# Optimization experiments

Hardware: AMD Instinct MI355X
Metric: run time of the kernel (lower is better)

## Reference

```python
import jax, jax.numpy as jnp
import numpy as np
from jax import lax

B, T = 64, 200
NUM_C, DIM_S, SIZE_M = 2000, 128, 50


def setup_inputs() -> dict:
    key = jax.random.key(0)
    ks = jax.random.split(key, 12)
    d = {}
    d['skill'] = jax.random.randint(ks[0], (B, T), 0, NUM_C)
    d['answer'] = jax.random.randint(ks[1], (B, T), 0, 2)
    s = 1.0 / np.sqrt(DIM_S)
    d['k_emb'] = jax.random.normal(ks[2], (NUM_C + 1, DIM_S), jnp.float32)
    d['v_emb'] = jax.random.normal(ks[3], (2 * NUM_C + 1, DIM_S), jnp.float32)
    # kaiming_normal on [size_m, dim_s]: std = sqrt(2/dim_s)
    d['Mk'] = jax.random.normal(ks[4], (SIZE_M, DIM_S), jnp.float32) * np.sqrt(2.0 / DIM_S)
    d['Mv0'] = jax.random.normal(ks[5], (SIZE_M, DIM_S), jnp.float32) * np.sqrt(2.0 / DIM_S)
    d['f_W'] = jax.random.normal(ks[6], (DIM_S, 2 * DIM_S), jnp.float32) * (1.0 / np.sqrt(2 * DIM_S))
    d['f_b'] = jnp.zeros((DIM_S,), jnp.float32)
    d['p_W'] = jax.random.normal(ks[7], (NUM_C, DIM_S), jnp.float32) * s
    d['p_b'] = jnp.zeros((NUM_C,), jnp.float32)
    d['e_W'] = jax.random.normal(ks[8], (DIM_S, DIM_S), jnp.float32) * s
    d['e_b'] = jnp.zeros((DIM_S,), jnp.float32)
    d['a_W'] = jax.random.normal(ks[9], (DIM_S, DIM_S), jnp.float32) * s
    d['a_b'] = jnp.zeros((DIM_S,), jnp.float32)
    return d


def reference(skill, answer, k_emb, v_emb, Mk, Mv0, f_W, f_b, p_W, p_b, e_W, e_b, a_W, a_b):
    num_c = p_W.shape[0]
    bsz = skill.shape[0]
    answer_x = jnp.where(answer == 2, 1, answer)
    x = skill + num_c * answer_x                       # [B,T]
    k = k_emb[skill]                                   # [B,T,D]
    v = v_emb[x]                                       # [B,T,D]
    w = jax.nn.softmax(jnp.einsum('btd,md->btm', k, Mk), axis=-1)   # [B,T,M]
    e = jax.nn.sigmoid(jnp.einsum('btd,ed->bte', v, e_W) + e_b)      # [B,T,D]
    a = jnp.tanh(jnp.einsum('btd,ed->bte', v, a_W) + a_b)            # [B,T,D]

    Mv_init = jnp.broadcast_to(Mv0, (bsz,) + Mv0.shape)              # [B,M,D]

    def step(Mvt, inp):
        et, at, wt = inp                               # [B,D],[B,D],[B,M]
        # read uses pre-update memory (Mv[:, :-1] in the torch code)
        read = jnp.einsum('bm,bmd->bd', wt, Mvt)
        Mvt_new = Mvt * (1.0 - wt[:, :, None] * et[:, None, :]) + wt[:, :, None] * at[:, None, :]
        return Mvt_new, read

    _, reads = lax.scan(step, Mv_init,
                        (e.transpose(1, 0, 2), a.transpose(1, 0, 2), w.transpose(1, 0, 2)))
    reads = reads.transpose(1, 0, 2)                   # [B,T,D]

    f = jnp.tanh(jnp.concatenate([reads, k], axis=-1) @ f_W.T + f_b)  # [B,T,D]
    p = jax.nn.sigmoid(f @ p_W.T + p_b)                # [B,T,num_c] (dropout is identity at eval)
    p = p[:, :-1, :]
    next_skill = skill[:, 1:]                          # [B,T-1]
    idx = jnp.minimum(next_skill, num_c - 1)
    pred = jnp.take_along_axis(p, idx[..., None], axis=-1)[..., 0]
    pred = jnp.where(next_skill < num_c, pred, 0.0)    # index num_c -> zero row in torch one_hot
    return pred
```

## Files before the change

kernel.cpp:

```cpp
#include <hip/hip_runtime.h>
#include <math.h>

#define Bsz 64
#define Tn 200
#define NUMC 2000
#define DS 128
#define SM 50
#define NTOK (Bsz*Tn)
#define WG2 10
#define MPG2 5

typedef __attribute__((ext_vector_type(8))) short bfrag;
typedef __attribute__((ext_vector_type(4))) float f32x4;
typedef __attribute__((ext_vector_type(4))) unsigned int u32x4;

__device__ __forceinline__ unsigned short f2bf(float x) {
    unsigned int u = __builtin_bit_cast(unsigned int, x);
    u = u + 0x7fffu + ((u >> 16) & 1u);
    return (unsigned short)(u >> 16);
}
__device__ __forceinline__ unsigned int pack2(float a, float b) {
    return (unsigned int)f2bf(a) | ((unsigned int)f2bf(b) << 16);
}
__device__ __forceinline__ bfrag mk_frag(f32x4 x, f32x4 y) {
    u32x4 t;
    t[0] = pack2(x[0], x[1]); t[1] = pack2(x[2], x[3]);
    t[2] = pack2(y[0], y[1]); t[3] = pack2(y[2], y[3]);
    return __builtin_bit_cast(bfrag, t);
}

__device__ __forceinline__ float fast_exp(float x)  { return __builtin_amdgcn_exp2f(x * 1.44269504f); }
__device__ __forceinline__ float fast_rcp(float x)  { return __builtin_amdgcn_rcpf(x); }
__device__ __forceinline__ float fast_sigmoid(float x) { return fast_rcp(1.f + fast_exp(-x)); }
__device__ __forceinline__ float fast_tanh(float x) { return 1.f - 2.f * fast_rcp(fast_exp(2.f * x) + 1.f); }

__device__ __forceinline__ void load_group(const bfrag* __restrict__ B, int nt0, int L, bfrag bf[4][4]) {
    #pragma unroll
    for (int t = 0; t < 4; t++)
        #pragma unroll
        for (int ki = 0; ki < 4; ki++)
            bf[t][ki] = B[(size_t)((nt0 + t) * 4 + ki) * 64 + L];
}
__device__ __forceinline__ void mfma_group(const bfrag A[4], const bfrag bf[4][4], f32x4 acc[4]) {
    #pragma unroll
    for (int ki = 0; ki < 4; ki++)
        #pragma unroll
        for (int t = 0; t < 4; t++)
            acc[t] = __builtin_amdgcn_mfma_f32_16x16x32_bf16(A[ki], bf[t][ki], acc[t], 0, 0, 0);
}

__global__ __launch_bounds__(256) void k0_cast(
    const float* __restrict__ eW, const float* __restrict__ aW,
    const float* __restrict__ fW, const float* __restrict__ Mk,
    unsigned int* __restrict__ BeaU, unsigned int* __restrict__ BkmU,
    unsigned int* __restrict__ Bf0U)
{
    const int g = blockIdx.x * 256 + threadIdx.x;
    if (g >= 9216) return;
    int gm, mat;
    unsigned int* dst;
    if (g < 4096)      { mat = 0; gm = g;        dst = BeaU; }
    else if (g < 7168) { mat = 1; gm = g - 4096; dst = BkmU; }
    else               { mat = 2; gm = g - 7168; dst = Bf0U; }
    const int nt = gm >> 8, r = gm & 255, ki = r >> 6, L = r & 63;
    const int n = nt * 16 + (L & 15);
    const int k = ki * 32 + (L >> 4) * 8;

    const float* src = nullptr;
    if (mat == 0) {
        src = (n < 128) ? (eW + (size_t)n * DS + k) : (aW + (size_t)(n - 128) * DS + k);
    } else if (mat == 1) {
        if (n < 128)      src = fW + (size_t)n * (2 * DS) + DS + k;
        else if (n < 128 + SM) src = Mk + (size_t)(n - 128) * DS + k;
    } else {
        src = fW + (size_t)n * (2 * DS) + k;
    }
    float v[8];
    #pragma unroll
    for (int j = 0; j < 8; j++) v[j] = src ? src[j] : 0.f;
    u32x4 o;
    o[0] = pack2(v[0], v[1]); o[1] = pack2(v[2], v[3]);
    o[2] = pack2(v[4], v[5]); o[3] = pack2(v[6], v[7]);
    ((u32x4*)dst)[gm] = o;
}

__global__ __launch_bounds__(64) void k1_gemm(
    const int* __restrict__ skill, const int* __restrict__ answer,
    const float* __restrict__ k_emb, const float* __restrict__ v_emb,
    const unsigned int* __restrict__ BeaU, const unsigned int* __restrict__ BkmU,
    const float* __restrict__ eB, const float* __restrict__ aB,
    float* __restrict__ w_buf, float* __restrict__ e_buf,
    float* __restrict__ a_buf, float* __restrict__ kp_buf)
{
    const int bid = blockIdx.x;
    const int L = threadIdx.x, L15 = L & 15, quad = L >> 4;

    if (bid < NTOK/16) {
        const int tok0 = bid * 16;
        const int tokA = tok0 + L15;
        const int tokD0 = tok0 + quad * 4;

        const bfrag* Bea = (const bfrag*)BeaU;
        bfrag bfA[4][4], bfB[4][4];
        load_group(Bea, 0, L, bfA);
        load_group(Bea, 4, L, bfB);

        const int s  = skill[tokA];
        const int an = answer[tokA];
        const int ax = (an == 2) ? 1 : an;
        const float* vp = v_emb + ((size_t)(s + NUMC * ax)) * DS + quad * 8;
        bfrag Vf[4];
        #pragma unroll
        for (int ki = 0; ki < 4; ki++) {
            const f32x4* a = (const f32x4*)(vp + ki * 32);
            Vf[ki] = mk_frag(a[0], a[1]);
        }

        f32x4 acc[4];
        #pragma unroll
        for (int t = 0; t < 4; t++) acc[t] = (f32x4){0.f,0.f,0.f,0.f};
        mfma_group(Vf, bfA, acc);
        load_group(Bea, 8, L, bfA);
        #pragma unroll
        for (int t = 0; t < 4; t++) {
            const int n = t * 16 + L15;
            const float bias = eB[n];
            #pragma unroll
            for (int reg = 0; reg < 4; reg++)
                e_buf[(size_t)(tokD0 + reg) * DS + n] = fast_sigmoid(acc[t][reg] + bias);
        }

        #pragma unroll
        for (int t = 0; t < 4; t++) acc[t] = (f32x4){0.f,0.f,0.f,0.f};
        mfma_group(Vf, bfB, acc);
        load_group(Bea, 12, L, bfB);
        #pragma unroll
        for (int t = 0; t < 4; t++) {
            const int n = (4 + t) * 16 + L15;
            const float bias = eB[n];
            #pragma unroll
            for (int reg = 0; reg < 4; reg++)
                e_buf[(size_t)(tokD0 + reg) * DS + n] = fast_sigmoid(acc[t][reg] + bias);
        }

        #pragma unroll
        for (int t = 0; t < 4; t++) acc[t] = (f32x4){0.f,0.f,0.f,0.f};
        mfma_group(Vf, bfA, acc);
        #pragma unroll
        for (int t = 0; t < 4; t++) {
            const int n = t * 16 + L15;
            const float bias = aB[n];
            #pragma unroll
            for (int reg = 0; reg < 4; reg++)
                a_buf[(size_t)(tokD0 + reg) * DS + n] = fast_tanh(acc[t][reg] + bias);
        }

        #pragma unroll
        for (int t = 0; t < 4; t++) acc[t] = (f32x4){0.f,0.f,0.f,0.f};
        mfma_group(Vf, bfB, acc);
        #pragma unroll
        for (int t = 0; t < 4; t++) {
            const int n = (4 + t) * 16 + L15;
            const float bias = aB[n];
            #pragma unroll
            for (int reg = 0; reg < 4; reg++)
                a_buf[(size_t)(tokD0 + reg) * DS + n] = fast_tanh(acc[t][reg] + bias);
        }
    } else {
        const int tok0 = (bid - NTOK/16) * 16;
        const int tokA = tok0 + L15;
        const int tokD0 = tok0 + quad * 4;

        const bfrag* Bkm = (const bfrag*)BkmU;
        bfrag bfA[4][4], bfB[4][4];
        load_group(Bkm, 0, L, bfA);
        load_group(Bkm, 4, L, bfB);

        const int s = skill[tokA];
        const float* kp = k_emb + (size_t)s * DS + quad * 8;
        bfrag Kf[4];
        #pragma unroll
        for (int ki = 0; ki < 4; ki++) {
            const f32x4* b = (const f32x4*)(kp + ki * 32);
            Kf[ki] = mk_frag(b[0], b[1]);
        }

        __shared__ float wl[16][52];

        f32x4 acc[4];
        #pragma unroll
        for (int t = 0; t < 4; t++) acc[t] = (f32x4){0.f,0.f,0.f,0.f};
        mfma_group(Kf, bfA, acc);
        load_group(Bkm, 8, L, bfA);
        #pragma unroll
        for (int t = 0; t < 4; t++) {
            const int n = t * 16 + L15;
            #pragma unroll
            for (int reg = 0; reg < 4; reg++)
                kp_buf[(size_t)(tokD0 + reg) * DS + n] = acc[t][reg];
        }

        #pragma unroll
        for (int t = 0; t < 4; t++) acc[t] = (f32x4){0.f,0.f,0.f,0.f};
        mfma_group(Kf, bfB, acc);
        #pragma unroll
        for (int t = 0; t < 4; t++) {
            const int n = (4 + t) * 16 + L15;
            #pragma unroll
            for (int reg = 0; reg < 4; reg++)
                kp_buf[(size_t)(tokD0 + reg) * DS + n] = acc[t][reg];
        }

        #pragma unroll
        for (int t = 0; t < 4; t++) acc[t] = (f32x4){0.f,0.f,0.f,0.f};
        mfma_group(Kf, bfA, acc);
        #pragma unroll
        for (int t = 0; t < 4; t++) {
            const int c = (8 + t) * 16 + L15 - 128;
            if (c < SM) {
                #pragma unroll
                for (int reg = 0; reg < 4; reg++)
                    wl[quad * 4 + reg][c] = acc[t][reg];
            }
        }
        __syncthreads();
        if (L < 16) {
            float mx = -1e30f;
            for (int m = 0; m < SM; m++) mx = fmaxf(mx, wl[L][m]);
            float sum = 0.f;
            float ex[SM];
            for (int m = 0; m < SM; m++) { ex[m] = fast_exp(wl[L][m] - mx); sum += ex[m]; }
            const float inv = fast_rcp(sum);
            float* wp = w_buf + (size_t)(tok0 + L) * SM;
            for (int m = 0; m < SM; m++) wp[m] = ex[m] * inv;
        }
    }
}

__global__ __launch_bounds__(64) void k2_scan(
    const float* __restrict__ w_buf, const float* __restrict__ e_buf,
    const float* __restrict__ a_buf, const float* __restrict__ Mv0,
    float* __restrict__ part_buf)
{
    const int bi   = blockIdx.x;
    const int b    = bi / (2*WG2);
    const int r    = bi % (2*WG2);
    const int dh   = r / WG2;
    const int mg   = r % WG2;
    const int lane = threadIdx.x;
    const int d    = dh*64 + lane;
    const int m0   = mg * MPG2;
    const int base = b * Tn;

    float Mv[MPG2];
    #pragma unroll
    for (int m = 0; m < MPG2; m++) Mv[m] = Mv0[(size_t)(m0+m)*DS + d];

    float* pout = part_buf + (size_t)mg * NTOK * DS;

    float se[4][2], sa[4][2], sw[4][2][MPG2];

    #define LOADST(ST, T)                                                      \
        { const int tc_ = ((T) < Tn) ? (T) : 0;                                \
          _Pragma("unroll")                                                    \
          for (int q_ = 0; q_ < 2; q_++) {                                     \
              const int tf_ = base + tc_ + q_;                                 \
              se[ST][q_] = e_buf[(size_t)tf_*DS + d];                          \
              sa[ST][q_] = a_buf[(size_t)tf_*DS + d];                          \
              _Pragma("unroll")                                                \
              for (int m_ = 0; m_ < MPG2; m_++)                                \
                  sw[ST][q_][m_] = w_buf[(size_t)tf_*SM + m0 + m_];            \
          } }

    LOADST(0, 0) LOADST(1, 2) LOADST(2, 4) LOADST(3, 6)

    for (int i = 0; i < 25; i++) {
        const int tb = i * 8;
        #pragma unroll
        for (int sub = 0; sub < 4; sub++) {
            const int t0 = tb + sub * 2;
            #pragma unroll
            for (int q = 0; q < 2; q++) {
                const float ev = se[sub][q], av = sa[sub][q];
                float rd = 0.f;
                #pragma unroll
                for (int m = 0; m < MPG2; m++) {
                    const float wm = sw[sub][q][m];
                    rd = fmaf(wm, Mv[m], rd);
                    Mv[m] = fmaf(-wm, fmaf(ev, Mv[m], -av), Mv[m]);
                }
                pout[(size_t)(base + t0 + q)*DS + d] = rd;
            }
            LOADST(sub, t0 + 8)
        }
    }
}

__global__ __launch_bounds__(64) void k3_gemm(
    const float* __restrict__ part_buf, const float* __restrict__ kp_buf,
    const unsigned int* __restrict__ Bf0U, const float* __restrict__ fB,
    const float* __restrict__ pW, const float* __restrict__ pB,
    const int* __restrict__ skill, float* __restrict__ out)
{
    const int L = threadIdx.x, L15 = L & 15, quad = L >> 4;
    const int tok0 = blockIdx.x * 16;
    const int tokA = tok0 + L15;
    const int tokD0 = tok0 + quad * 4;

    const bfrag* Bf0 = (const bfrag*)Bf0U;
    bfrag bfA[4][4], bfB[4][4];
    load_group(Bf0, 0, L, bfA);
    load_group(Bf0, 4, L, bfB);

    bfrag Rf[4];
    #pragma unroll
    for (int ki = 0; ki < 4; ki++) {
        const float* p0 = part_buf + (size_t)tokA * DS + ki * 32 + quad * 8;
        f32x4 x = (f32x4){0.f,0.f,0.f,0.f}, y = (f32x4){0.f,0.f,0.f,0.f};
        #pragma unroll
        for (int g = 0; g < WG2; g++) {
            const f32x4* q4 = (const f32x4*)(p0 + (size_t)g * NTOK * DS);
            x = x + q4[0]; y = y + q4[1];
        }
        Rf[ki] = mk_frag(x, y);
    }

    float f[4][8];
    f32x4 acc[4];

    #pragma unroll
    for (int t = 0; t < 4; t++) acc[t] = (f32x4){0.f,0.f,0.f,0.f};
    mfma_group(Rf, bfA, acc);
    #pragma unroll
    for (int t = 0; t < 4; t++) {
        const int n = t * 16 + L15;
        const float fb = fB[n];
        #pragma unroll
        for (int reg = 0; reg < 4; reg++)
            f[reg][t] = fast_tanh(acc[t][reg] + kp_buf[(size_t)(tokD0 + reg) * DS + n] + fb);
    }

    #pragma unroll
    for (int t = 0; t < 4; t++) acc[t] = (f32x4){0.f,0.f,0.f,0.f};
    mfma_group(Rf, bfB, acc);
    #pragma unroll
    for (int t = 0; t < 4; t++) {
        const int n = (4 + t) * 16 + L15;
        const float fb = fB[n];
        #pragma unroll
        for (int reg = 0; reg < 4; reg++)
            f[reg][4 + t] = fast_tanh(acc[t][reg] + kp_buf[(size_t)(tokD0 + reg) * DS + n] + fb);
    }

    #pragma unroll
    for (int reg = 0; reg < 4; reg++) {
        const int tok = tokD0 + reg;
        const int t = tok % Tn;
        const bool act = (t < Tn - 1);
        int sn = 0, ix = 0;
        float contrib = 0.f;
        if (act) {
            sn = skill[tok + 1];
            ix = (sn < NUMC) ? sn : (NUMC - 1);
            const float* pr = pW + (size_t)ix * DS + L15;
            #pragma unroll
            for (int nt = 0; nt < 8; nt++)
                contrib = fmaf(f[reg][nt], pr[nt * 16], contrib);
        }
        #pragma unroll
        for (int msk = 1; msk <= 8; msk <<= 1)
            contrib += __shfl_xor(contrib, msk);
        if (act && L15 == 0) {
            const float val = contrib + pB[ix];
            const float prd = (sn < NUMC) ? fast_sigmoid(val) : 0.f;
            out[(size_t)(tok / Tn) * (Tn - 1) + t] = prd;
        }
    }
}

extern "C" void kernel_launch(void* const* d_in, const int* in_sizes, int n_in,
                              void* d_out, int out_size, void* d_ws, size_t ws_size,
                              hipStream_t stream)
{
    const int*   skill  = (const int*)  d_in[0];
    const int*   answer = (const int*)  d_in[1];
    const float* k_emb  = (const float*)d_in[2];
    const float* v_emb  = (const float*)d_in[3];
    const float* Mk     = (const float*)d_in[4];
    const float* Mv0    = (const float*)d_in[5];
    const float* f_W    = (const float*)d_in[6];
    const float* f_b    = (const float*)d_in[7];
    const float* p_W    = (const float*)d_in[8];
    const float* p_b    = (const float*)d_in[9];
    const float* e_W    = (const float*)d_in[10];
    const float* e_b    = (const float*)d_in[11];
    const float* a_W    = (const float*)d_in[12];
    const float* a_b    = (const float*)d_in[13];
    float* out = (float*)d_out;

    float* ws       = (float*)d_ws;
    float* w_buf    = ws;
    float* e_buf    = w_buf    + (size_t)NTOK*SM;
    float* a_buf    = e_buf    + (size_t)NTOK*DS;
    float* kp_buf   = a_buf    + (size_t)NTOK*DS;
    float* part_buf = kp_buf   + (size_t)NTOK*DS;
    unsigned int* BeaU = (unsigned int*)(part_buf + (size_t)WG2*NTOK*DS);
    unsigned int* BkmU = BeaU + 4096 * 4;
    unsigned int* Bf0U = BkmU + 3072 * 4;

    k0_cast<<<36, 256, 0, stream>>>(e_W, a_W, f_W, Mk, BeaU, BkmU, Bf0U);
    k1_gemm<<<2*(NTOK/16), 64, 0, stream>>>(skill, answer, k_emb, v_emb,
        BeaU, BkmU, e_b, a_b, w_buf, e_buf, a_buf, kp_buf);
    k2_scan<<<Bsz*2*WG2, 64, 0, stream>>>(w_buf, e_buf, a_buf, Mv0, part_buf);
    k3_gemm<<<NTOK/16, 64, 0, stream>>>(part_buf, kp_buf, Bf0U, f_b,
        p_W, p_b, skill, out);
}
```

Before: 140.6 us.

## Reduce scan partial reads in shared memory instead of global partial buffer

The scan kernel now packs the 10 memory-slot groups as waves of one workgroup (640 threads per batch/half) and sums their per-step read contributions through a shared-memory stash every 20 steps. Only the final reads go to global memory, so the 10x partial buffer and the 10-way reduction in the output GEMM kernel are gone. In exchange the scan gains two __syncthreads per chunk, which couple the waves, and there are fewer, larger workgroups, which may hurt latency hiding.

```diff
diff --git a/kernel.cpp b/kernel.cpp
--- a/kernel.cpp
+++ b/kernel.cpp
@@ -7,8 +7,9 @@
 #define DS 128
 #define SM 50
 #define NTOK (Bsz*Tn)
-#define WG2 10
-#define MPG2 5
+#define MPG 5
+#define NWV 10
+#define CH 20
 
 typedef __attribute__((ext_vector_type(8))) short bfrag;
 typedef __attribute__((ext_vector_type(4))) float f32x4;
@@ -237,28 +238,26 @@
     }
 }
 
-__global__ __launch_bounds__(64) void k2_scan(
+__global__ __launch_bounds__(64*NWV) void k2_scan(
     const float* __restrict__ w_buf, const float* __restrict__ e_buf,
     const float* __restrict__ a_buf, const float* __restrict__ Mv0,
-    float* __restrict__ part_buf)
+    float* __restrict__ reads_buf)
 {
-    const int bi   = blockIdx.x;
-    const int b    = bi / (2*WG2);
-    const int r    = bi % (2*WG2);
-    const int dh   = r / WG2;
-    const int mg   = r % WG2;
-    const int lane = threadIdx.x;
-    const int d    = dh*64 + lane;
-    const int m0   = mg * MPG2;
+    const int b    = blockIdx.x >> 1;
+    const int dh   = blockIdx.x & 1;
+    const int wave = threadIdx.x >> 6;
+    const int lane = threadIdx.x & 63;
+    const int d    = dh * 64 + lane;
+    const int m0   = wave * MPG;
     const int base = b * Tn;
 
-    float Mv[MPG2];
-    #pragma unroll
-    for (int m = 0; m < MPG2; m++) Mv[m] = Mv0[(size_t)(m0+m)*DS + d];
-
-    float* pout = part_buf + (size_t)mg * NTOK * DS;
-
-    float se[4][2], sa[4][2], sw[4][2][MPG2];
+    __shared__ float stash[NWV][CH][64];
+
+    float Mv[MPG];
+    #pragma unroll
+    for (int m = 0; m < MPG; m++) Mv[m] = Mv0[(size_t)(m0+m)*DS + d];
+
+    float se[4][2], sa[4][2], sw[4][2][MPG];
 
     #define LOADST(ST, T)                                                      \
         { const int tc_ = ((T) < Tn) ? (T) : 0;                                \
@@ -268,36 +267,48 @@
               se[ST][q_] = e_buf[(size_t)tf_*DS + d];                          \
               sa[ST][q_] = a_buf[(size_t)tf_*DS + d];                          \
               _Pragma("unroll")                                                \
-              for (int m_ = 0; m_ < MPG2; m_++)                                \
+              for (int m_ = 0; m_ < MPG; m_++)                                 \
                   sw[ST][q_][m_] = w_buf[(size_t)tf_*SM + m0 + m_];            \
           } }
 
     LOADST(0, 0) LOADST(1, 2) LOADST(2, 4) LOADST(3, 6)
 
-    for (int i = 0; i < 25; i++) {
-        const int tb = i * 8;
-        #pragma unroll
-        for (int sub = 0; sub < 4; sub++) {
-            const int t0 = tb + sub * 2;
+    for (int c = 0; c < Tn/CH; c++) {
+        #pragma unroll
+        for (int s = 0; s < CH/2; s++) {
+            const int t0 = c*CH + s*2;
+            const int st = (c*(CH/2) + s) & 3;
             #pragma unroll
             for (int q = 0; q < 2; q++) {
-                const float ev = se[sub][q], av = sa[sub][q];
+                const float ev = se[st][q], av = sa[st][q];
                 float rd = 0.f;
                 #pragma unroll
-                for (int m = 0; m < MPG2; m++) {
-                    const float wm = sw[sub][q][m];
+                for (int m = 0; m < MPG; m++) {
+                    const float wm = sw[st][q][m];
                     rd = fmaf(wm, Mv[m], rd);
                     Mv[m] = fmaf(-wm, fmaf(ev, Mv[m], -av), Mv[m]);
                 }
-                pout[(size_t)(base + t0 + q)*DS + d] = rd;
+                stash[wave][s*2+q][lane] = rd;
             }
-            LOADST(sub, t0 + 8)
-        }
-    }
+            LOADST(st, t0 + 8)
+        }
+        __syncthreads();
+        #pragma unroll
+        for (int q = 0; q < 2; q++) {
+            const int slot = threadIdx.x + q * (64*NWV);
+            const int tl = slot >> 6, dl = slot & 63;
+            float sum = 0.f;
+            #pragma unroll
+            for (int g = 0; g < NWV; g++) sum += stash[g][tl][dl];
+            reads_buf[(size_t)(base + c*CH + tl)*DS + dh*64 + dl] = sum;
+        }
+        __syncthreads();
+    }
+    #undef LOADST
 }
 
 __global__ __launch_bounds__(64) void k3_gemm(
-    const float* __restrict__ part_buf, const float* __restrict__ kp_buf,
+    const float* __restrict__ reads_buf, const float* __restrict__ kp_buf,
     const unsigned int* __restrict__ Bf0U, const float* __restrict__ fB,
     const float* __restrict__ pW, const float* __restrict__ pB,
     const int* __restrict__ skill, float* __restrict__ out)
@@ -315,14 +326,8 @@
     bfrag Rf[4];
     #pragma unroll
     for (int ki = 0; ki < 4; ki++) {
-        const float* p0 = part_buf + (size_t)tokA * DS + ki * 32 + quad * 8;
-        f32x4 x = (f32x4){0.f,0.f,0.f,0.f}, y = (f32x4){0.f,0.f,0.f,0.f};
-        #pragma unroll
-        for (int g = 0; g < WG2; g++) {
-            const f32x4* q4 = (const f32x4*)(p0 + (size_t)g * NTOK * DS);
-            x = x + q4[0]; y = y + q4[1];
-        }
-        Rf[ki] = mk_frag(x, y);
+        const f32x4* q4 = (const f32x4*)(reads_buf + (size_t)tokA * DS + ki * 32 + quad * 8);
+        Rf[ki] = mk_frag(q4[0], q4[1]);
     }
 
     float f[4][8];
@@ -398,20 +403,20 @@
     const float* a_b    = (const float*)d_in[13];
     float* out = (float*)d_out;
 
-    float* ws       = (float*)d_ws;
-    float* w_buf    = ws;
-    float* e_buf    = w_buf    + (size_t)NTOK*SM;
-    float* a_buf    = e_buf    + (size_t)NTOK*DS;
-    float* kp_buf   = a_buf    + (size_t)NTOK*DS;
-    float* part_buf = kp_buf   + (size_t)NTOK*DS;
-    unsigned int* BeaU = (unsigned int*)(part_buf + (size_t)WG2*NTOK*DS);
+    float* ws        = (float*)d_ws;
+    float* w_buf     = ws;
+    float* e_buf     = w_buf     + (size_t)NTOK*SM;
+    float* a_buf     = e_buf     + (size_t)NTOK*DS;
+    float* kp_buf    = a_buf     + (size_t)NTOK*DS;
+    float* reads_buf = kp_buf    + (size_t)NTOK*DS;
+    unsigned int* BeaU = (unsigned int*)(reads_buf + (size_t)NTOK*DS);
     unsigned int* BkmU = BeaU + 4096 * 4;
     unsigned int* Bf0U = BkmU + 3072 * 4;
 
     k0_cast<<<36, 256, 0, stream>>>(e_W, a_W, f_W, Mk, BeaU, BkmU, Bf0U);
     k1_gemm<<<2*(NTOK/16), 64, 0, stream>>>(skill, answer, k_emb, v_emb,
         BeaU, BkmU, e_b, a_b, w_buf, e_buf, a_buf, kp_buf);
-    k2_scan<<<Bsz*2*WG2, 64, 0, stream>>>(w_buf, e_buf, a_buf, Mv0, part_buf);
-    k3_gemm<<<NTOK/16, 64, 0, stream>>>(part_buf, kp_buf, Bf0U, f_b,
+    k2_scan<<<Bsz*2, 64*NWV, 0, stream>>>(w_buf, e_buf, a_buf, Mv0, reads_buf);
+    k3_gemm<<<NTOK/16, 64, 0, stream>>>(reads_buf, kp_buf, Bf0U, f_b,
         p_W, p_b, skill, out);
 }
```

Result: slower. 294.8 us (+109.7%).

## Drop weight pre-cast kernel and store scan partial reads in bf16

Applied to the files above, without the earlier changes.

Removes the k0_cast launch that pre-packed weights into bf16 fragment layout. Each GEMM block now loads fp32 weights directly and converts them in registers. The scan kernel also writes its 10 per-group partial read sums as bf16 instead of fp32, halving that intermediate traffic, and k3 widens and sums them. This saves a launch and a large chunk of workspace bandwidth, at the cost of redundant per-block weight conversion, twice the weight load bytes, and some precision lost on the partial sums.

```diff
diff --git a/kernel.cpp b/kernel.cpp
--- a/kernel.cpp
+++ b/kernel.cpp
@@ -22,6 +22,9 @@
 __device__ __forceinline__ unsigned int pack2(float a, float b) {
     return (unsigned int)f2bf(a) | ((unsigned int)f2bf(b) << 16);
 }
+__device__ __forceinline__ float bf2f(unsigned int u) {
+    return __builtin_bit_cast(float, u << 16);
+}
 __device__ __forceinline__ bfrag mk_frag(f32x4 x, f32x4 y) {
     u32x4 t;
     t[0] = pack2(x[0], x[1]); t[1] = pack2(x[2], x[3]);
@@ -34,12 +37,53 @@
 __device__ __forceinline__ float fast_sigmoid(float x) { return fast_rcp(1.f + fast_exp(-x)); }
 __device__ __forceinline__ float fast_tanh(float x) { return 1.f - 2.f * fast_rcp(fast_exp(2.f * x) + 1.f); }
 
-__device__ __forceinline__ void load_group(const bfrag* __restrict__ B, int nt0, int L, bfrag bf[4][4]) {
-    #pragma unroll
-    for (int t = 0; t < 4; t++)
-        #pragma unroll
-        for (int ki = 0; ki < 4; ki++)
-            bf[t][ki] = B[(size_t)((nt0 + t) * 4 + ki) * 64 + L];
+__device__ __forceinline__ void load_group_ea(
+    const float* __restrict__ eW, const float* __restrict__ aW,
+    int nt0, int L15, int quad, bfrag bf[4][4])
+{
+    #pragma unroll
+    for (int t = 0; t < 4; t++) {
+        const int n = (nt0 + t) * 16 + L15;
+        const float* row = (n < 128) ? (eW + (size_t)n * DS) : (aW + (size_t)(n - 128) * DS);
+        #pragma unroll
+        for (int ki = 0; ki < 4; ki++) {
+            const float* p = row + ki * 32 + quad * 8;
+            bf[t][ki] = mk_frag(*(const f32x4*)p, *(const f32x4*)(p + 4));
+        }
+    }
+}
+__device__ __forceinline__ void load_group_km(
+    const float* __restrict__ fW, const float* __restrict__ Mk,
+    int nt0, int L15, int quad, bfrag bf[4][4])
+{
+    #pragma unroll
+    for (int t = 0; t < 4; t++) {
+        const int n = (nt0 + t) * 16 + L15;
+        const bool valid = n < 128 + SM;
+        const float* row = (n < 128) ? (fW + (size_t)n * (2*DS) + DS)
+                                     : (Mk + (size_t)(n - 128) * DS);
+        #pragma unroll
+        for (int ki = 0; ki < 4; ki++) {
+            const float* p = row + ki * 32 + quad * 8;
+            f32x4 x = valid ? *(const f32x4*)p       : (f32x4){0.f,0.f,0.f,0.f};
+            f32x4 y = valid ? *(const f32x4*)(p + 4) : (f32x4){0.f,0.f,0.f,0.f};
+            bf[t][ki] = mk_frag(x, y);
+        }
+    }
+}
+__device__ __forceinline__ void load_group_f0(
+    const float* __restrict__ fW, int nt0, int L15, int quad, bfrag bf[4][4])
+{
+    #pragma unroll
+    for (int t = 0; t < 4; t++) {
+        const int n = (nt0 + t) * 16 + L15;
+        const float* row = fW + (size_t)n * (2*DS);
+        #pragma unroll
+        for (int ki = 0; ki < 4; ki++) {
+            const float* p = row + ki * 32 + quad * 8;
+            bf[t][ki] = mk_frag(*(const f32x4*)p, *(const f32x4*)(p + 4));
+        }
+    }
 }
 __device__ __forceinline__ void mfma_group(const bfrag A[4], const bfrag bf[4][4], f32x4 acc[4]) {
     #pragma unroll
@@ -47,47 +91,13 @@
         #pragma unroll
         for (int t = 0; t < 4; t++)
             acc[t] = __builtin_amdgcn_mfma_f32_16x16x32_bf16(A[ki], bf[t][ki], acc[t], 0, 0, 0);
-}
-
-__global__ __launch_bounds__(256) void k0_cast(
-    const float* __restrict__ eW, const float* __restrict__ aW,
-    const float* __restrict__ fW, const float* __restrict__ Mk,
-    unsigned int* __restrict__ BeaU, unsigned int* __restrict__ BkmU,
-    unsigned int* __restrict__ Bf0U)
-{
-    const int g = blockIdx.x * 256 + threadIdx.x;
-    if (g >= 9216) return;
-    int gm, mat;
-    unsigned int* dst;
-    if (g < 4096)      { mat = 0; gm = g;        dst = BeaU; }
-    else if (g < 7168) { mat = 1; gm = g - 4096; dst = BkmU; }
-    else               { mat = 2; gm = g - 7168; dst = Bf0U; }
-    const int nt = gm >> 8, r = gm & 255, ki = r >> 6, L = r & 63;
-    const int n = nt * 16 + (L & 15);
-    const int k = ki * 32 + (L >> 4) * 8;
-
-    const float* src = nullptr;
-    if (mat == 0) {
-        src = (n < 128) ? (eW + (size_t)n * DS + k) : (aW + (size_t)(n - 128) * DS + k);
-    } else if (mat == 1) {
-        if (n < 128)      src = fW + (size_t)n * (2 * DS) + DS + k;
-        else if (n < 128 + SM) src = Mk + (size_t)(n - 128) * DS + k;
-    } else {
-        src = fW + (size_t)n * (2 * DS) + k;
-    }
-    float v[8];
-    #pragma unroll
-    for (int j = 0; j < 8; j++) v[j] = src ? src[j] : 0.f;
-    u32x4 o;
-    o[0] = pack2(v[0], v[1]); o[1] = pack2(v[2], v[3]);
-    o[2] = pack2(v[4], v[5]); o[3] = pack2(v[6], v[7]);
-    ((u32x4*)dst)[gm] = o;
 }
 
 __global__ __launch_bounds__(64) void k1_gemm(
     const int* __restrict__ skill, const int* __restrict__ answer,
     const float* __restrict__ k_emb, const float* __restrict__ v_emb,
-    const unsigned int* __restrict__ BeaU, const unsigned int* __restrict__ BkmU,
+    const float* __restrict__ eW, const float* __restrict__ aW,
+    const float* __restrict__ fW, const float* __restrict__ Mk,
     const float* __restrict__ eB, const float* __restrict__ aB,
     float* __restrict__ w_buf, float* __restrict__ e_buf,
     float* __restrict__ a_buf, float* __restrict__ kp_buf)
@@ -100,10 +110,9 @@
         const int tokA = tok0 + L15;
         const int tokD0 = tok0 + quad * 4;
 
-        const bfrag* Bea = (const bfrag*)BeaU;
         bfrag bfA[4][4], bfB[4][4];
-        load_group(Bea, 0, L, bfA);
-        load_group(Bea, 4, L, bfB);
+        load_group_ea(eW, aW, 0, L15, quad, bfA);
+        load_group_ea(eW, aW, 4, L15, quad, bfB);
 
         const int s  = skill[tokA];
         const int an = answer[tokA];
@@ -120,7 +129,7 @@
         #pragma unroll
         for (int t = 0; t < 4; t++) acc[t] = (f32x4){0.f,0.f,0.f,0.f};
         mfma_group(Vf, bfA, acc);
-        load_group(Bea, 8, L, bfA);
+        load_group_ea(eW, aW, 8, L15, quad, bfA);
         #pragma unroll
         for (int t = 0; t < 4; t++) {
             const int n = t * 16 + L15;
@@ -133,7 +142,7 @@
         #pragma unroll
         for (int t = 0; t < 4; t++) acc[t] = (f32x4){0.f,0.f,0.f,0.f};
         mfma_group(Vf, bfB, acc);
-        load_group(Bea, 12, L, bfB);
+        load_group_ea(eW, aW, 12, L15, quad, bfB);
         #pragma unroll
         for (int t = 0; t < 4; t++) {
             const int n = (4 + t) * 16 + L15;
@@ -171,10 +180,9 @@
         const int tokA = tok0 + L15;
         const int tokD0 = tok0 + quad * 4;
 
-        const bfrag* Bkm = (const bfrag*)BkmU;
         bfrag bfA[4][4], bfB[4][4];
-        load_group(Bkm, 0, L, bfA);
-        load_group(Bkm, 4, L, bfB);
+        load_group_km(fW, Mk, 0, L15, quad, bfA);
+        load_group_km(fW, Mk, 4, L15, quad, bfB);
 
         const int s = skill[tokA];
         const float* kp = k_emb + (size_t)s * DS + quad * 8;
@@ -191,7 +199,7 @@
         #pragma unroll
         for (int t = 0; t < 4; t++) acc[t] = (f32x4){0.f,0.f,0.f,0.f};
         mfma_group(Kf, bfA, acc);
-        load_group(Bkm, 8, L, bfA);
+        load_group_km(fW, Mk, 8, L15, quad, bfA);
         #pragma unroll
         for (int t = 0; t < 4; t++) {
             const int n = t * 16 + L15;
@@ -240,7 +248,7 @@
 __global__ __launch_bounds__(64) void k2_scan(
     const float* __restrict__ w_buf, const float* __restrict__ e_buf,
     const float* __restrict__ a_buf, const float* __restrict__ Mv0,
-    float* __restrict__ part_buf)
+    unsigned short* __restrict__ part16)
 {
     const int bi   = blockIdx.x;
     const int b    = bi / (2*WG2);
@@ -256,7 +264,7 @@
     #pragma unroll
     for (int m = 0; m < MPG2; m++) Mv[m] = Mv0[(size_t)(m0+m)*DS + d];
 
-    float* pout = part_buf + (size_t)mg * NTOK * DS;
+    unsigned short* pout = part16 + (size_t)mg * NTOK * DS;
 
     float se[4][2], sa[4][2], sw[4][2][MPG2];
 
@@ -289,16 +297,17 @@
                     rd = fmaf(wm, Mv[m], rd);
                     Mv[m] = fmaf(-wm, fmaf(ev, Mv[m], -av), Mv[m]);
                 }
-                pout[(size_t)(base + t0 + q)*DS + d] = rd;
+                pout[(size_t)(base + t0 + q)*DS + d] = f2bf(rd);
             }
             LOADST(sub, t0 + 8)
         }
     }
+    #undef LOADST
 }
 
 __global__ __launch_bounds__(64) void k3_gemm(
-    const float* __restrict__ part_buf, const float* __restrict__ kp_buf,
-    const unsigned int* __restrict__ Bf0U, const float* __restrict__ fB,
+    const unsigned short* __restrict__ part16, const float* __restrict__ kp_buf,
+    const float* __restrict__ fW, const float* __restrict__ fB,
     const float* __restrict__ pW, const float* __restrict__ pB,
     const int* __restrict__ skill, float* __restrict__ out)
 {
@@ -307,22 +316,24 @@
     const int tokA = tok0 + L15;
     const int tokD0 = tok0 + quad * 4;
 
-    const bfrag* Bf0 = (const bfrag*)Bf0U;
     bfrag bfA[4][4], bfB[4][4];
-    load_group(Bf0, 0, L, bfA);
-    load_group(Bf0, 4, L, bfB);
+    load_group_f0(fW, 0, L15, quad, bfA);
+    load_group_f0(fW, 4, L15, quad, bfB);
 
     bfrag Rf[4];
     #pragma unroll
     for (int ki = 0; ki < 4; ki++) {
-        const float* p0 = part_buf + (size_t)tokA * DS + ki * 32 + quad * 8;
-        f32x4 x = (f32x4){0.f,0.f,0.f,0.f}, y = (f32x4){0.f,0.f,0.f,0.f};
+        const unsigned short* p0 = part16 + (size_t)tokA * DS + ki * 32 + quad * 8;
+        float s0=0,s1=0,s2=0,s3=0,s4=0,s5=0,s6=0,s7=0;
         #pragma unroll
         for (int g = 0; g < WG2; g++) {
-            const f32x4* q4 = (const f32x4*)(p0 + (size_t)g * NTOK * DS);
-            x = x + q4[0]; y = y + q4[1];
-        }
-        Rf[ki] = mk_frag(x, y);
+            u32x4 v = *(const u32x4*)(p0 + (size_t)g * NTOK * DS);
+            s0 += bf2f(v[0] & 0xffffu); s1 += bf2f(v[0] >> 16);
+            s2 += bf2f(v[1] & 0xffffu); s3 += bf2f(v[1] >> 16);
+            s4 += bf2f(v[2] & 0xffffu); s5 += bf2f(v[2] >> 16);
+            s6 += bf2f(v[3] & 0xffffu); s7 += bf2f(v[3] >> 16);
+        }
+        Rf[ki] = mk_frag((f32x4){s0,s1,s2,s3}, (f32x4){s4,s5,s6,s7});
     }
 
     float f[4][8];
@@ -398,20 +409,16 @@
     const float* a_b    = (const float*)d_in[13];
     float* out = (float*)d_out;
 
-    float* ws       = (float*)d_ws;
-    float* w_buf    = ws;
-    float* e_buf    = w_buf    + (size_t)NTOK*SM;
-    float* a_buf    = e_buf    + (size_t)NTOK*DS;
-    float* kp_buf   = a_buf    + (size_t)NTOK*DS;
-    float* part_buf = kp_buf   + (size_t)NTOK*DS;
-    unsigned int* BeaU = (unsigned int*)(part_buf + (size_t)WG2*NTOK*DS);
-    unsigned int* BkmU = BeaU + 4096 * 4;
-    unsigned int* Bf0U = BkmU + 3072 * 4;
-
-    k0_cast<<<36, 256, 0, stream>>>(e_W, a_W, f_W, Mk, BeaU, BkmU, Bf0U);
+    float* ws     = (float*)d_ws;
+    float* w_buf  = ws;
+    float* e_buf  = w_buf  + (size_t)NTOK*SM;
+    float* a_buf  = e_buf  + (size_t)NTOK*DS;
+    float* kp_buf = a_buf  + (size_t)NTOK*DS;
+    unsigned short* part16 = (unsigned short*)(kp_buf + (size_t)NTOK*DS);
+
     k1_gemm<<<2*(NTOK/16), 64, 0, stream>>>(skill, answer, k_emb, v_emb,
-        BeaU, BkmU, e_b, a_b, w_buf, e_buf, a_buf, kp_buf);
-    k2_scan<<<Bsz*2*WG2, 64, 0, stream>>>(w_buf, e_buf, a_buf, Mv0, part_buf);
-    k3_gemm<<<NTOK/16, 64, 0, stream>>>(part_buf, kp_buf, Bf0U, f_b,
+        e_W, a_W, f_W, Mk, e_b, a_b, w_buf, e_buf, a_buf, kp_buf);
+    k2_scan<<<Bsz*2*WG2, 64, 0, stream>>>(w_buf, e_buf, a_buf, Mv0, part16);
+    k3_gemm<<<NTOK/16, 64, 0, stream>>>(part16, kp_buf, f_W, f_b,
         p_W, p_b, skill, out);
 }
```

Result: slower. 172.4 us (+22.6%).
